# Kernel optimization log

Hardware: AMD Instinct MI355X
Metric: run time of the kernel (lower is better)

The kernel has to match this reference:

```python
import jax, jax.numpy as jnp
import numpy as np

UNITS = 14336
IN_FEATURES = 4096
PACKED = IN_FEATURES // 4  # 4 ternary values (2 bits each) per byte
CLIP_VAL = 100.0

# 2-bit crumb -> ternary value lookup: 0 -> 0, 1 -> +1, 2 -> -1, 3 -> 0
_TERNARY_LUT = jnp.array([0.0, 1.0, -1.0, 0.0], dtype=jnp.float32)


def _unpack_ternary(pw):
    """pw: [U, P] int (byte values 0..255) -> dense ternary float W [U, 4*P].
    Little-endian crumbs within each byte (shifts 0,2,4,6)."""
    crumbs = jnp.stack([(pw >> (2 * i)) & 3 for i in range(4)], axis=-1)  # [U, P, 4]
    crumbs = crumbs.reshape(pw.shape[0], -1)  # [U, 4*P]
    return _TERNARY_LUT[crumbs][:, :IN_FEATURES]  # [U, IN]


def setup_inputs() -> dict:
    key = jax.random.key(0)
    k1, k2, k3, k4 = jax.random.split(key, 4)
    x = jax.random.normal(k1, (32, IN_FEATURES), dtype=jnp.float32)
    # packed ternary weights, one uint8-valued byte per 4 ternary weights
    pw = jax.random.randint(k2, (UNITS, PACKED), 0, 256, dtype=jnp.int32)
    scale = 1.0 + 0.02 * jax.random.normal(k3, (UNITS,), dtype=jnp.float32)
    bias = 0.01 * jax.random.normal(k4, (UNITS,), dtype=jnp.float32)
    return {"x": x, "pw": pw, "scale": scale, "bias": bias}


def reference(x, pw, scale, bias):
    # dense ternary weight [UNITS, IN]; kernel target would fuse this unpack into the GEMM
    W = _unpack_ternary(pw)
    y = jnp.einsum('bd,ud->bu', x, W)  # [B, UNITS]
    y = y * scale + bias               # per-unit affine dequant
    return jnp.clip(y, -CLIP_VAL, CLIP_VAL)
```

## Files before the change

kernel.cpp:

```cpp
#include <hip/hip_runtime.h>

#define UNITS 14336
#define IN_F 4096
#define PACKED 1024
#define CLIP_VAL 100.0f

typedef unsigned int uint32;

using bf16x8 = __attribute__((ext_vector_type(8))) short;
using f32x4  = __attribute__((ext_vector_type(4))) float;

__device__ inline unsigned short f2bf(float f) {
    uint32 u = __float_as_uint(f);
    u += 0x7FFFu + ((u >> 16) & 1u);
    return (unsigned short)(u >> 16);
}

__device__ inline uint32 pack2bf(float a, float b) {
    return (uint32)f2bf(a) | ((uint32)f2bf(b) << 16);
}

__device__ inline void unpack_byte(uint32 v, uint32& r0, uint32& r1) {
    uint32 t0 = (v & 3u) | ((v & 0xCu) << 14);
    uint32 t1 = ((v >> 4) & 3u) | ((v & 0xC0u) << 10);
    uint32 s0 = t0 >> 1;
    uint32 s1 = t1 >> 1;
    uint32 nz0 = (t0 ^ s0) & 0x00010001u;
    uint32 nz1 = (t1 ^ s1) & 0x00010001u;
    r0 = nz0 * 0x3F80u + ((s0 & 0x00010001u) << 15);
    r1 = nz1 * 0x3F80u + ((s1 & 0x00010001u) << 15);
}

__device__ inline float clipf(float y) {
    return fminf(fmaxf(y, -CLIP_VAL), CLIP_VAL);
}


__global__ __launch_bounds__(256) void convert_x_kernel(
    const float* __restrict__ x, uint4* __restrict__ ws) {
    int t = blockIdx.x * 256 + threadIdx.x;
    int lane = t & 63;
    int h = (t >> 6) & 1;
    int s = (t >> 7) & 1;
    int g = t >> 8;
    int n = lane & 15;
    int q = lane >> 4;
    int b = h * 16 + n;
    int k0 = g * 64 + q * 16 + s * 8;
    const float4* src = (const float4*)(x + (size_t)b * IN_F + k0);
    float4 lo = src[0];
    float4 hi = src[1];
    uint4 o;
    o.x = pack2bf(lo.x, lo.y);
    o.y = pack2bf(lo.z, lo.w);
    o.z = pack2bf(hi.x, hi.y);
    o.w = pack2bf(hi.z, hi.w);
    ws[t] = o;
}

__global__ __launch_bounds__(512, 8) void ternary_mm_kernel(
    const uint4* __restrict__ xw,
    const int*   __restrict__ pw,
    const float* __restrict__ scale,
    const float* __restrict__ bias,
    float*       __restrict__ out) {
    __shared__ char  stg[16 * 1040];
    __shared__ f32x4 red[8][2][64];

    const int tid  = threadIdx.x;
    const int wid  = tid >> 6;
    const int lane = tid & 63;
    const int q    = lane >> 4;
    const int n    = lane & 15;
    const int u0   = blockIdx.x << 4;
    const int g0   = wid << 3;

    {
        const char* src = (const char*)pw;
        #pragma unroll
        for (int j = 0; j < 8; ++j) {
            const int j2 = j >> 1;
            const int hh = j & 1;
            const int row = (j2 << 2) + q;
            const int cc  = (wid << 5) + (hh << 4) + n;
            uint4 v = *(const uint4*)(src + (size_t)(u0 + row) * 4096
                                          + ((size_t)cc << 4));
            uint32 d = (v.x & 0xFFu) | ((v.y & 0xFFu) << 8)
                     | ((v.z & 0xFFu) << 16) | ((v.w & 0xFFu) << 24);
            *(uint32*)(stg + row * 1040 + (cc << 2)) = d;
        }
    }

    const uint4* xb = xw + (g0 << 8) + lane;
    const char*  lb = stg + n * 1040 + (((wid << 5) + q) << 2);

    f32x4 acc0 = {0.f,0.f,0.f,0.f};
    f32x4 acc1 = {0.f,0.f,0.f,0.f};

    #pragma unroll
    for (int i = 0; i < 8; ++i) {
        uint4 x00 = xb[(i << 8)];
        uint4 x01 = xb[(i << 8) + 64];
        uint4 x10 = xb[(i << 8) + 128];
        uint4 x11 = xb[(i << 8) + 192];
        uint32 w = *(const uint32*)(lb + (i << 4));

        uint4 fA, fB;
        unpack_byte(w & 0xFFu,         fA.x, fA.y);
        unpack_byte((w >> 8) & 0xFFu,  fA.z, fA.w);
        unpack_byte((w >> 16) & 0xFFu, fB.x, fB.y);
        unpack_byte(w >> 24,           fB.z, fB.w);
        bf16x8 vA = __builtin_bit_cast(bf16x8, fA);
        bf16x8 vB = __builtin_bit_cast(bf16x8, fB);

        acc0 = __builtin_amdgcn_mfma_f32_16x16x32_bf16(
            __builtin_bit_cast(bf16x8, x00), vA, acc0, 0, 0, 0);
        acc1 = __builtin_amdgcn_mfma_f32_16x16x32_bf16(
            __builtin_bit_cast(bf16x8, x01), vA, acc1, 0, 0, 0);
        acc0 = __builtin_amdgcn_mfma_f32_16x16x32_bf16(
            __builtin_bit_cast(bf16x8, x10), vB, acc0, 0, 0, 0);
        acc1 = __builtin_amdgcn_mfma_f32_16x16x32_bf16(
            __builtin_bit_cast(bf16x8, x11), vB, acc1, 0, 0, 0);
    }

    red[wid][0][lane] = acc0;
    red[wid][1][lane] = acc1;
    __syncthreads();

    if (tid < 128) {
        const int h = tid >> 6;
        const int l = tid & 63;
        f32x4 s = red[0][h][l];
        #pragma unroll
        for (int w = 1; w < 8; ++w) {
            f32x4 v = red[w][h][l];
            s[0] += v[0]; s[1] += v[1]; s[2] += v[2]; s[3] += v[3];
        }
        const int u  = u0 + (l & 15);
        const int b0 = h * 16 + ((l >> 4) << 2);
        const float sc = scale[u];
        const float bi = bias[u];
        float* o = out + (size_t)b0 * UNITS + u;
        o[0 * UNITS] = clipf(s[0] * sc + bi);
        o[1 * UNITS] = clipf(s[1] * sc + bi);
        o[2 * UNITS] = clipf(s[2] * sc + bi);
        o[3 * UNITS] = clipf(s[3] * sc + bi);
    }
}

extern "C" void kernel_launch(void* const* d_in, const int* in_sizes, int n_in,
                              void* d_out, int out_size, void* d_ws, size_t ws_size,
                              hipStream_t stream) {
    const float* x     = (const float*)d_in[0];
    const int*   pw    = (const int*)d_in[1];
    const float* scale = (const float*)d_in[2];
    const float* bias  = (const float*)d_in[3];
    float* out = (float*)d_out;

    uint4* xw = (uint4*)d_ws;

    convert_x_kernel<<<64, 256, 0, stream>>>(x, xw);
    ternary_mm_kernel<<<UNITS / 16, 512, 0, stream>>>(xw, pw, scale, bias, out);
}
```

Before: 104.1 us.

## Switch to 32x32x16 MFMA with 32-unit tiles per block

```diff
diff --git a/kernel.cpp b/kernel.cpp
--- a/kernel.cpp
+++ b/kernel.cpp
@@ -8,7 +8,7 @@
 typedef unsigned int uint32;
 
 using bf16x8 = __attribute__((ext_vector_type(8))) short;
-using f32x4  = __attribute__((ext_vector_type(4))) float;
+using f32x16 = __attribute__((ext_vector_type(16))) float;
 
 __device__ inline unsigned short f2bf(float f) {
     uint32 u = __float_as_uint(f);
@@ -40,14 +40,12 @@
     const float* __restrict__ x, uint4* __restrict__ ws) {
     int t = blockIdx.x * 256 + threadIdx.x;
     int lane = t & 63;
-    int h = (t >> 6) & 1;
-    int s = (t >> 7) & 1;
-    int g = t >> 8;
-    int n = lane & 15;
-    int q = lane >> 4;
-    int b = h * 16 + n;
-    int k0 = g * 64 + q * 16 + s * 8;
-    const float4* src = (const float4*)(x + (size_t)b * IN_F + k0);
+    int s = (t >> 6) & 1;
+    int G = t >> 7;
+    int n = lane & 31;
+    int p = lane >> 5;
+    int k0 = G * 32 + p * 16 + s * 8;
+    const float4* src = (const float4*)(x + (size_t)n * IN_F + k0);
     float4 lo = src[0];
     float4 hi = src[1];
     uint4 o;
@@ -64,87 +62,81 @@
     const float* __restrict__ scale,
     const float* __restrict__ bias,
     float*       __restrict__ out) {
-    __shared__ char  stg[16 * 1040];
-    __shared__ f32x4 red[8][2][64];
+    __shared__ uint32 lds4[8448];
+    char* lds = (char*)lds4;
 
     const int tid  = threadIdx.x;
     const int wid  = tid >> 6;
     const int lane = tid & 63;
-    const int q    = lane >> 4;
-    const int n    = lane & 15;
-    const int u0   = blockIdx.x << 4;
-    const int g0   = wid << 3;
+    const int n32  = lane & 31;
+    const int p    = lane >> 5;
+    const int u0   = blockIdx.x << 5;
 
     {
         const char* src = (const char*)pw;
         #pragma unroll
-        for (int j = 0; j < 8; ++j) {
-            const int j2 = j >> 1;
-            const int hh = j & 1;
-            const int row = (j2 << 2) + q;
-            const int cc  = (wid << 5) + (hh << 4) + n;
+        for (int j = 0; j < 16; ++j) {
+            const int row = ((j & 7) << 2) + (lane >> 4);
+            const int c   = (wid << 5) + ((j >> 3) << 4) + (lane & 15);
             uint4 v = *(const uint4*)(src + (size_t)(u0 + row) * 4096
-                                          + ((size_t)cc << 4));
+                                          + ((size_t)c << 4));
             uint32 d = (v.x & 0xFFu) | ((v.y & 0xFFu) << 8)
                      | ((v.z & 0xFFu) << 16) | ((v.w & 0xFFu) << 24);
-            *(uint32*)(stg + row * 1040 + (cc << 2)) = d;
+            *(uint32*)(lds + row * 1028 + (c << 2)) = d;
         }
     }
 
-    const uint4* xb = xw + (g0 << 8) + lane;
-    const char*  lb = stg + n * 1040 + (((wid << 5) + q) << 2);
+    f32x16 acc = {0.f,0.f,0.f,0.f,0.f,0.f,0.f,0.f,
+                  0.f,0.f,0.f,0.f,0.f,0.f,0.f,0.f};
 
-    f32x4 acc0 = {0.f,0.f,0.f,0.f};
-    f32x4 acc1 = {0.f,0.f,0.f,0.f};
+    const char*  lb = lds + n32 * 1028 + ((((wid << 5)) + p) << 2);
+    const uint4* xg = xw + ((wid << 4) << 7) + lane;
 
     #pragma unroll
-    for (int i = 0; i < 8; ++i) {
-        uint4 x00 = xb[(i << 8)];
-        uint4 x01 = xb[(i << 8) + 64];
-        uint4 x10 = xb[(i << 8) + 128];
-        uint4 x11 = xb[(i << 8) + 192];
-        uint32 w = *(const uint32*)(lb + (i << 4));
+    for (int ig = 0; ig < 16; ++ig) {
+        uint32 w = *(const uint32*)(lb + (ig << 3));
+        uint4 x0 = xg[(ig << 7)];
+        uint4 x1 = xg[(ig << 7) + 64];
 
         uint4 fA, fB;
         unpack_byte(w & 0xFFu,         fA.x, fA.y);
         unpack_byte((w >> 8) & 0xFFu,  fA.z, fA.w);
         unpack_byte((w >> 16) & 0xFFu, fB.x, fB.y);
         unpack_byte(w >> 24,           fB.z, fB.w);
-        bf16x8 vA = __builtin_bit_cast(bf16x8, fA);
-        bf16x8 vB = __builtin_bit_cast(bf16x8, fB);
 
-        acc0 = __builtin_amdgcn_mfma_f32_16x16x32_bf16(
-            __builtin_bit_cast(bf16x8, x00), vA, acc0, 0, 0, 0);
-        acc1 = __builtin_amdgcn_mfma_f32_16x16x32_bf16(
-            __builtin_bit_cast(bf16x8, x01), vA, acc1, 0, 0, 0);
-        acc0 = __builtin_amdgcn_mfma_f32_16x16x32_bf16(
-            __builtin_bit_cast(bf16x8, x10), vB, acc0, 0, 0, 0);
-        acc1 = __builtin_amdgcn_mfma_f32_16x16x32_bf16(
-            __builtin_bit_cast(bf16x8, x11), vB, acc1, 0, 0, 0);
+        acc = __builtin_amdgcn_mfma_f32_32x32x16_bf16(
+            __builtin_bit_cast(bf16x8, fA),
+            __builtin_bit_cast(bf16x8, x0), acc, 0, 0, 0);
+        acc = __builtin_amdgcn_mfma_f32_32x32x16_bf16(
+            __builtin_bit_cast(bf16x8, fB),
+            __builtin_bit_cast(bf16x8, x1), acc, 0, 0, 0);
     }
 
-    red[wid][0][lane] = acc0;
-    red[wid][1][lane] = acc1;
+    __syncthreads();
+    {
+        float* red = (float*)lds4;
+        float4* dst = (float4*)(red + lane * 132 + (wid << 4));
+        dst[0] = make_float4(acc[0],  acc[1],  acc[2],  acc[3]);
+        dst[1] = make_float4(acc[4],  acc[5],  acc[6],  acc[7]);
+        dst[2] = make_float4(acc[8],  acc[9],  acc[10], acc[11]);
+        dst[3] = make_float4(acc[12], acc[13], acc[14], acc[15]);
+    }
     __syncthreads();
 
-    if (tid < 128) {
-        const int h = tid >> 6;
-        const int l = tid & 63;
-        f32x4 s = red[0][h][l];
+    const float* red = (const float*)lds4;
+    #pragma unroll
+    for (int e0 = 0; e0 < 2; ++e0) {
+        const int e  = (e0 << 9) + tid;
+        const int lp = e >> 4;
+        const int r  = e & 15;
+        float s = 0.f;
         #pragma unroll
-        for (int w = 1; w < 8; ++w) {
-            f32x4 v = red[w][h][l];
-            s[0] += v[0]; s[1] += v[1]; s[2] += v[2]; s[3] += v[3];
-        }
-        const int u  = u0 + (l & 15);
-        const int b0 = h * 16 + ((l >> 4) << 2);
-        const float sc = scale[u];
-        const float bi = bias[u];
-        float* o = out + (size_t)b0 * UNITS + u;
-        o[0 * UNITS] = clipf(s[0] * sc + bi);
-        o[1 * UNITS] = clipf(s[1] * sc + bi);
-        o[2 * UNITS] = clipf(s[2] * sc + bi);
-        o[3 * UNITS] = clipf(s[3] * sc + bi);
+        for (int w = 0; w < 8; ++w)
+            s += red[lp * 132 + (w << 4) + r];
+        const int m  = (r & 3) + ((r >> 2) << 3) + ((lp >> 5) << 2);
+        const int nb = lp & 31;
+        const int u  = u0 + m;
+        out[(size_t)nb * UNITS + u] = clipf(s * scale[u] + bias[u]);
     }
 }
 
@@ -160,5 +152,5 @@
     uint4* xw = (uint4*)d_ws;
 
     convert_x_kernel<<<64, 256, 0, stream>>>(x, xw);
-    ternary_mm_kernel<<<UNITS / 16, 512, 0, stream>>>(xw, pw, scale, bias, out);
+    ternary_mm_kernel<<<UNITS / 32, 512, 0, stream>>>(xw, pw, scale, bias, out);
 }
```

Result: no change. 104.3 us (+0.1%).
